# Kernel tuning notes

Measured on AMD Instinct MI355X. Metric: run time of the kernel, lower is better.

## Reference

```python
import jax, jax.numpy as jnp
import numpy as np

C = 256          # channels
NH = 8           # heads
DH = 64          # dim_head
NMEM = 4         # num_mem_kv
HIDDEN = NH * DH # 512
SCALE = DH ** (-0.5)


def _rmsnorm(x, gain):
    # F.normalize(x, dim=1) * gain * sqrt(C)  (scale-only RMS norm over channel dim)
    n = jnp.sqrt(jnp.sum(x * x, axis=1, keepdims=True))
    return x / jnp.maximum(n, 1e-12) * gain * (x.shape[1] ** 0.5)


def setup_inputs() -> dict:
    key = jax.random.key(0)
    ks = jax.random.split(key, 6)
    B, Hh, Ww = 16, 64, 64
    return {
        "x": jax.random.normal(ks[0], (B, C, Hh, Ww), jnp.float32),
        "gain1": jnp.ones((1, C, 1, 1), jnp.float32),
        "w_qkv": jax.random.normal(ks[1], (3 * HIDDEN, C), jnp.float32) * 0.02,
        "mem_kv": jax.random.normal(ks[2], (2, NH, DH, NMEM), jnp.float32),
        "w_out": jax.random.normal(ks[3], (C, HIDDEN), jnp.float32) * 0.02,
        "b_out": jnp.zeros((C,), jnp.float32),
        "gain2": jnp.ones((1, C, 1, 1), jnp.float32),
    }


def reference(x, gain1, w_qkv, mem_kv, w_out, b_out, gain2):
    B, _, Hh, Ww = x.shape
    N = Hh * Ww
    # pre-norm
    xn = _rmsnorm(x, gain1)
    # 1x1 conv QKV projection (no bias) == channel GEMM
    qkv = jnp.einsum('oc,bchw->bohw', w_qkv, xn)          # [B, 3*hidden, H, W]
    qkv = qkv.reshape(B, 3, NH, DH, N)                    # chunk + 'b (h c) x y -> b h c (x y)'
    q, k, v = qkv[:, 0], qkv[:, 1], qkv[:, 2]             # [B, h, d, N]
    # learned global memory kv, broadcast over batch
    mem_k = jnp.broadcast_to(mem_kv[0], (B, NH, DH, NMEM))
    mem_v = jnp.broadcast_to(mem_kv[1], (B, NH, DH, NMEM))
    k = jnp.concatenate([mem_k, k], axis=-1)              # [B, h, d, NMEM+N]
    v = jnp.concatenate([mem_v, v], axis=-1)
    # dual softmax: q over feature dim d, k over token dim n
    q = jax.nn.softmax(q, axis=-2) * SCALE
    k = jax.nn.softmax(k, axis=-1)
    # linear attention: O(N) context
    context = jnp.einsum('bhdn,bhen->bhde', k, v)         # [B, h, d, e]
    out = jnp.einsum('bhde,bhdn->bhen', context, q)       # [B, h, e, N]
    out = out.reshape(B, HIDDEN, Hh, Ww)
    # 1x1 conv out projection (with bias) + post RMSNorm
    out = jnp.einsum('oc,bchw->bohw', w_out, out) + b_out[None, :, None, None]
    return _rmsnorm(out, gain2)
```

## Files before the change

### kernel.cpp

```cpp
#include <hip/hip_runtime.h>

typedef __attribute__((ext_vector_type(8))) short bf16x8;
typedef __attribute__((ext_vector_type(4))) short bf16x4;
typedef __attribute__((ext_vector_type(4))) float f32x4;
typedef unsigned short u16;

constexpr int B_   = 16;
constexpr int C_   = 256;
constexpr int NH   = 8;
constexpr int DH   = 64;
constexpr int NMEM = 4;
constexpr int HID  = 512;
constexpr int QKVC = 1536;
constexpr int N_   = 4096;
constexpr int CTXS = 4224;

__device__ __forceinline__ u16 f2b(float f) {
  union { float f; unsigned u; } v{f};
  unsigned r = v.u + 0x7fff + ((v.u >> 16) & 1);
  return (u16)(r >> 16);
}
__device__ __forceinline__ float b2f(u16 h) {
  union { unsigned u; float f; } v; v.u = ((unsigned)h) << 16; return v.f;
}

__device__ __forceinline__ void gld_lds16(const u16* g, u16* l) {
  __builtin_amdgcn_global_load_lds(
      (const __attribute__((address_space(1))) unsigned*)g,
      (__attribute__((address_space(3))) unsigned*)l, 16, 0, 0);
}

__global__ void k_cvtw(const float* __restrict__ wq, const float* __restrict__ wo,
                       u16* __restrict__ wqb, u16* __restrict__ wob) {
  int i = blockIdx.x * 256 + threadIdx.x;
  for (int idx = i; idx < QKVC * C_; idx += gridDim.x * 256) wqb[idx] = f2b(wq[idx]);
  for (int idx = i; idx < C_ * HID; idx += gridDim.x * 256) wob[idx] = f2b(wo[idx]);
}

__global__ __launch_bounds__(256) void k_rms1(const float* __restrict__ x,
                                              const float* __restrict__ g1,
                                              u16* __restrict__ xbT) {
  int g = blockIdx.y;
  int n = blockIdx.x * 64 + (threadIdx.x & 63);
  int ch = threadIdx.x >> 6;
  __shared__ float ssp[4][64];
  __shared__ float invs[64];
  const float* xp = x + (size_t)g * C_ * N_ + n;
  float ss = 0.f;
  #pragma unroll 16
  for (int c = ch * 64; c < ch * 64 + 64; ++c) {
    float v = xp[(size_t)c * N_];
    ss += v * v;
  }
  ssp[ch][n & 63] = ss;
  __syncthreads();
  if (threadIdx.x < 64) {
    float tot = (ssp[0][threadIdx.x] + ssp[1][threadIdx.x]) +
                (ssp[2][threadIdx.x] + ssp[3][threadIdx.x]);
    invs[threadIdx.x] = 16.0f / fmaxf(sqrtf(tot), 1e-12f);
  }
  __syncthreads();
  float inv = invs[n & 63];
  u16* op = xbT + ((size_t)g * N_ + n) * C_;
  #pragma unroll 2
  for (int c0 = ch * 64; c0 < ch * 64 + 64; c0 += 8) {
    union { bf16x8 v; u16 u[8]; } pk;
    #pragma unroll
    for (int j = 0; j < 8; ++j) pk.u[j] = f2b(xp[(size_t)(c0 + j) * N_] * inv * g1[c0 + j]);
    *(bf16x8*)(op + c0) = pk.v;
  }
}

__global__ __launch_bounds__(256) void k_kvctx(const u16* __restrict__ Wb,
                                               const u16* __restrict__ XT,
                                               float* __restrict__ ctxp) {
  __shared__ __align__(16) u16 smem[16384];
  u16* Ws = smem;
  u16* Xs = smem + 8192;
  u16* Pl = smem;
  u16* Vl = smem + 8192;

  int cpx = gridDim.x >> 3;
  int bid = blockIdx.x;
  int L = (bid & 7) * cpx + (bid >> 3);
  int h = L & 7, nc = (L >> 3) & 7, g = L >> 6;
  int t = threadIdx.x, wave = t >> 6, lane = t & 63;
  int wm = wave >> 1, wn = wave & 1;
  int kg = lane >> 4, lr = lane & 15;

  const u16* WK = Wb + (size_t)(HID + h * DH) * C_;
  const u16* WV = Wb + (size_t)(2 * HID + h * DH) * C_;
  const u16* Xg = XT + ((size_t)g * N_ + nc * 512) * C_;

  int rl8 = lane >> 3;
  int cs8 = (lane & 7) ^ rl8;
  const u16* Wsrc = (wave < 2) ? WK : WV;

  f32x4 acc2[4];
  #pragma unroll
  for (int nf = 0; nf < 4; ++nf) acc2[nf] = (f32x4)0.f;
  float rs[4] = {0.f, 0.f, 0.f, 0.f};

  for (int it = 0; it < 4; ++it) {
    f32x4 acc[4][4];
    #pragma unroll
    for (int i = 0; i < 4; ++i)
      #pragma unroll
      for (int j = 0; j < 4; ++j) acc[i][j] = (f32x4)0.f;

    for (int k0 = 0; k0 < C_; k0 += 64) {
      #pragma unroll
      for (int q = 0; q < 4; ++q) {
        int rb = wave * 32 + q * 8;
        int rw = (rb & 63) + rl8;
        int rx = it * 128 + rb + rl8;
        gld_lds16(Wsrc + (size_t)rw * C_ + k0 + cs8 * 8, Ws + rb * 64);
        gld_lds16(Xg + (size_t)rx * C_ + k0 + cs8 * 8, Xs + rb * 64);
      }
      __syncthreads();
      #pragma unroll
      for (int ks = 0; ks < 2; ++ks) {
        int ch = ks * 4 + kg;
        bf16x8 a[4], bv[4];
        #pragma unroll
        for (int mf = 0; mf < 4; ++mf) {
          int r = wm * 64 + mf * 16 + lr;
          a[mf] = *(const bf16x8*)(Xs + r * 64 + ((ch ^ (r & 7)) * 8));
        }
        #pragma unroll
        for (int nf = 0; nf < 4; ++nf) {
          int r = wn * 64 + nf * 16 + lr;
          bv[nf] = *(const bf16x8*)(Ws + r * 64 + ((ch ^ (r & 7)) * 8));
        }
        #pragma unroll
        for (int mf = 0; mf < 4; ++mf)
          #pragma unroll
          for (int nf = 0; nf < 4; ++nf)
            acc[mf][nf] = __builtin_amdgcn_mfma_f32_16x16x32_bf16(a[mf], bv[nf], acc[mf][nf], 0, 0, 0);
      }
      __syncthreads();
    }

    if (wn == 0) {
      #pragma unroll
      for (int mf = 0; mf < 4; ++mf) {
        int nb = wm * 64 + mf * 16 + kg * 4;
        int cc = nb >> 3, off = nb & 7;
        #pragma unroll
        for (int nf = 0; nf < 4; ++nf) {
          int d = nf * 16 + lr;
          float e0 = __expf(acc[mf][nf][0]);
          float e1 = __expf(acc[mf][nf][1]);
          float e2 = __expf(acc[mf][nf][2]);
          float e3 = __expf(acc[mf][nf][3]);
          rs[nf] += (e0 + e1) + (e2 + e3);
          union { bf16x4 v; u16 u[4]; } pk;
          pk.u[0] = f2b(e0); pk.u[1] = f2b(e1); pk.u[2] = f2b(e2); pk.u[3] = f2b(e3);
          *(bf16x4*)(Pl + d * 128 + ((cc ^ (d & 15)) * 8) + off) = pk.v;
        }
      }
    } else {
      #pragma unroll
      for (int mf = 0; mf < 4; ++mf) {
        int nb = wm * 64 + mf * 16 + kg * 4;
        int cc = nb >> 3, off = nb & 7;
        #pragma unroll
        for (int nf = 0; nf < 4; ++nf) {
          int e = nf * 16 + lr;
          union { bf16x4 v; u16 u[4]; } pk;
          pk.u[0] = f2b(acc[mf][nf][0]); pk.u[1] = f2b(acc[mf][nf][1]);
          pk.u[2] = f2b(acc[mf][nf][2]); pk.u[3] = f2b(acc[mf][nf][3]);
          *(bf16x4*)(Vl + e * 128 + ((cc ^ (e & 15)) * 8) + off) = pk.v;
        }
      }
    }
    __syncthreads();

    #pragma unroll
    for (int k = 0; k < 4; ++k) {
      int c = k * 4 + kg;
      bf16x8 af = *(const bf16x8*)(Pl + (wave * 16 + lr) * 128 + ((c ^ lr) * 8));
      #pragma unroll
      for (int nf = 0; nf < 4; ++nf) {
        bf16x8 bfv = *(const bf16x8*)(Vl + (nf * 16 + lr) * 128 + ((c ^ lr) * 8));
        acc2[nf] = __builtin_amdgcn_mfma_f32_16x16x32_bf16(af, bfv, acc2[nf], 0, 0, 0);
      }
    }
    __syncthreads();
  }

  float* cgp = ctxp + ((size_t)(g * NH + h) * 8 + nc) * CTXS;
  #pragma unroll
  for (int nf = 0; nf < 4; ++nf)
    #pragma unroll
    for (int j = 0; j < 4; ++j) {
      int d = wave * 16 + kg * 4 + j;
      int e = nf * 16 + lr;
      cgp[d * 64 + e] = acc2[nf][j];
    }
  if (wn == 0) {
    #pragma unroll
    for (int nf = 0; nf < 4; ++nf) {
      rs[nf] += __shfl_xor(rs[nf], 16);
      rs[nf] += __shfl_xor(rs[nf], 32);
    }
    if (lane < 16) {
      #pragma unroll
      for (int nf = 0; nf < 4; ++nf)
        cgp[4096 + wm * 64 + nf * 16 + lane] = rs[nf];
    }
  }
}

__global__ __launch_bounds__(256) void k_cwo(const float* __restrict__ ctxp,
                                             const float* __restrict__ memkv,
                                             const u16* __restrict__ Wo,
                                             u16* __restrict__ wo2) {
  int g = blockIdx.y, h = blockIdx.x;
  int t = threadIdx.x, wave = t >> 6, lane = t & 63;
  int kg = lane >> 4, lr = lane & 15;
  int rl8 = lane >> 3, cs8 = (lane & 7) ^ rl8;
  __shared__ float emk[DH * NMEM];
  __shared__ float sd[DH];
  __shared__ __align__(16) u16 Cl[64 * 64];
  __shared__ __align__(16) u16 As2[256 * 64];

  const float* mk = memkv + (size_t)h * DH * NMEM;
  const float* mv = memkv + (size_t)(NH + h) * DH * NMEM;
  const float* cp = ctxp + (size_t)(g * NH + h) * 8 * CTXS;
  emk[t] = __expf(mk[t]);
  __syncthreads();
  if (t < DH) {
    float s = 0.f;
    #pragma unroll
    for (int p = 0; p < 8; ++p)
      s += cp[p * CTXS + 4096 + t] + cp[p * CTXS + 4160 + t];
    #pragma unroll
    for (int j = 0; j < NMEM; ++j) s += emk[t * 4 + j];
    sd[t] = s;
  }
  #pragma unroll
  for (int q = 0; q < 8; ++q) {
    int rb = wave * 64 + q * 8;
    gld_lds16(Wo + (size_t)(rb + rl8) * HID + h * DH + cs8 * 8, As2 + rb * 64);
  }
  __syncthreads();
  #pragma unroll
  for (int i = 0; i < 16; ++i) {
    int idx = t + 256 * i;
    int d = idx >> 6, e = idx & 63;
    float v = 0.f;
    #pragma unroll
    for (int p = 0; p < 8; ++p) v += cp[p * CTXS + idx];
    #pragma unroll
    for (int j = 0; j < NMEM; ++j) v += emk[d * 4 + j] * mv[e * 4 + j];
    Cl[d * 64 + (((e >> 3) ^ (d & 7)) * 8) + (e & 7)] = f2b(v / sd[d]);
  }
  __syncthreads();
  f32x4 acc[4][4];
  #pragma unroll
  for (int i = 0; i < 4; ++i)
    #pragma unroll
    for (int j = 0; j < 4; ++j) acc[i][j] = (f32x4)0.f;
  #pragma unroll
  for (int ks = 0; ks < 2; ++ks) {
    int ch = ks * 4 + kg;
    bf16x8 a[4], b[4];
    #pragma unroll
    for (int mf = 0; mf < 4; ++mf) {
      int r = wave * 64 + mf * 16 + lr;
      a[mf] = *(const bf16x8*)(As2 + r * 64 + ((ch ^ (r & 7)) * 8));
    }
    #pragma unroll
    for (int nf = 0; nf < 4; ++nf) {
      int rd = nf * 16 + lr;
      b[nf] = *(const bf16x8*)(Cl + rd * 64 + ((ch ^ (rd & 7)) * 8));
    }
    #pragma unroll
    for (int mf = 0; mf < 4; ++mf)
      #pragma unroll
      for (int nf = 0; nf < 4; ++nf)
        acc[mf][nf] = __builtin_amdgcn_mfma_f32_16x16x32_bf16(a[mf], b[nf], acc[mf][nf], 0, 0, 0);
  }
  u16* og = wo2 + (size_t)g * 256 * 512;
  #pragma unroll
  for (int mf = 0; mf < 4; ++mf)
    #pragma unroll
    for (int nf = 0; nf < 4; ++nf)
      #pragma unroll
      for (int j = 0; j < 4; ++j) {
        int c = wave * 64 + mf * 16 + kg * 4 + j;
        int dd = nf * 16 + lr;
        og[(size_t)c * 512 + h * DH + dd] = f2b(acc[mf][nf][j]);
      }
}

__global__ __launch_bounds__(512) void k_qout(const u16* __restrict__ Wq,
                                              const u16* __restrict__ XT,
                                              const u16* __restrict__ Wo2,
                                              const float* __restrict__ bias,
                                              const float* __restrict__ g2,
                                              float* __restrict__ out) {
  __shared__ __align__(16) u16 smem[49152];
  u16* R0 = smem;
  u16* R1 = smem + 16384;

  int cpx = gridDim.x >> 3;
  int bid = blockIdx.x;
  int L = (bid & 7) * cpx + (bid >> 3);
  int nc = L & 31, g = L >> 5;
  int t = threadIdx.x, wave = t >> 6, lane = t & 63;
  int kg = lane >> 4, lr = lane & 15;
  int rl4 = lane >> 2, cs4 = (lane & 3) ^ (rl4 & 3);
  int rl8 = lane >> 3, cs8 = (lane & 7) ^ rl8;

  const u16* Xg = XT + ((size_t)g * N_ + nc * 128) * C_;
  const u16* W2g = Wo2 + (size_t)g * 256 * 512;

  {
    int xrow_off = lane >> 5;
    int c32 = lane & 31;
    #pragma unroll
    for (int q = 0; q < 8; ++q) {
      int base = wave * 16 + q * 2;
      int row = base + xrow_off;
      int sw = (c32 & 24) | ((c32 & 7) ^ (row & 7));
      gld_lds16(Xg + (size_t)row * C_ + sw * 8, R1 + base * 256);
    }
  }

  f32x4 acc[4][8];
  #pragma unroll
  for (int i = 0; i < 4; ++i)
    #pragma unroll
    for (int j = 0; j < 8; ++j) acc[i][j] = (f32x4)0.f;

  for (int k0i = 0; k0i < 8; ++k0i) {
    int k0 = k0i * 32;
    #pragma unroll
    for (int q = 0; q < 4; ++q) {
      int rb = ((wave * 4 + q) & 31) * 16;
      gld_lds16(Wq + (size_t)(rb + rl4) * C_ + k0 + cs4 * 8, R0 + rb * 32);
    }
    __syncthreads();
    bf16x8 a[4], bv[8];
    #pragma unroll
    for (int mf = 0; mf < 4; ++mf) {
      int r = wave * 64 + mf * 16 + lr;
      a[mf] = *(const bf16x8*)(R0 + r * 32 + ((kg ^ (r & 3)) * 8));
    }
    #pragma unroll
    for (int nf = 0; nf < 8; ++nf) {
      int bn = nf * 16 + lr;
      int c32 = k0i * 4 + kg;
      int sw = (c32 & 24) | ((c32 & 7) ^ (bn & 7));
      bv[nf] = *(const bf16x8*)(R1 + bn * 256 + sw * 8);
    }
    #pragma unroll
    for (int mf = 0; mf < 4; ++mf)
      #pragma unroll
      for (int nf = 0; nf < 8; ++nf)
        acc[mf][nf] = __builtin_amdgcn_mfma_f32_16x16x32_bf16(a[mf], bv[nf], acc[mf][nf], 0, 0, 0);
    __syncthreads();
  }

  float colsum[8];
  #pragma unroll
  for (int nf = 0; nf < 8; ++nf) {
    float s = 0.f;
    #pragma unroll
    for (int mf = 0; mf < 4; ++mf)
      #pragma unroll
      for (int j = 0; j < 4; ++j) {
        float e = __expf(acc[mf][nf][j]);
        acc[mf][nf][j] = e;
        s += e;
      }
    colsum[nf] = s;
  }
  #pragma unroll
  for (int nf = 0; nf < 8; ++nf) {
    colsum[nf] += __shfl_xor(colsum[nf], 16);
    colsum[nf] += __shfl_xor(colsum[nf], 32);
    colsum[nf] = 0.125f / colsum[nf];
  }
  unsigned pq[4][8][2];
  #pragma unroll
  for (int nf = 0; nf < 8; ++nf) {
    float invs = colsum[nf];
    #pragma unroll
    for (int mf = 0; mf < 4; ++mf)
      #pragma unroll
      for (int jp = 0; jp < 2; ++jp) {
        u16 lo = f2b(acc[mf][nf][jp * 2] * invs);
        u16 hi = f2b(acc[mf][nf][jp * 2 + 1] * invs);
        pq[mf][nf][jp] = (unsigned)lo | ((unsigned)hi << 16);
      }
  }

  f32x4 acc2[2][8];
  #pragma unroll
  for (int i = 0; i < 2; ++i)
    #pragma unroll
    for (int j = 0; j < 8; ++j) acc2[i][j] = (f32x4)0.f;

  #pragma unroll
  for (int half = 0; half < 2; ++half) {
    if ((wave >> 2) == half) {
      #pragma unroll
      for (int nf = 0; nf < 8; ++nf) {
        int n = nf * 16 + lr;
        #pragma unroll
        for (int mf = 0; mf < 4; ++mf)
          #pragma unroll
          for (int jp = 0; jp < 2; ++jp) {
            int oc = (wave & 3) * 64 + mf * 16 + kg * 4 + jp * 2;
            int c8 = oc >> 3;
            int sw = (c8 & 24) | ((c8 & 7) ^ (n & 7));
            *(unsigned*)(R1 + n * 256 + sw * 8 + (oc & 7)) = pq[mf][nf][jp];
          }
      }
    }
    __syncthreads();
    for (int k0l = 0; k0l < 4; ++k0l) {
      int cb = half * 256 + k0l * 64;
      #pragma unroll
      for (int q = 0; q < 4; ++q) {
        int rb = ((wave * 4 + q) & 31) * 8;
        gld_lds16(W2g + (size_t)(rb + rl8) * 512 + cb + cs8 * 8, R0 + rb * 64);
      }
      __syncthreads();
      #pragma unroll
      for (int ks = 0; ks < 2; ++ks) {
        int ch = ks * 4 + kg;
        bf16x8 a2[2], b2[8];
        #pragma unroll
        for (int mf = 0; mf < 2; ++mf) {
          int r = wave * 32 + mf * 16 + lr;
          a2[mf] = *(const bf16x8*)(R0 + r * 64 + ((ch ^ (r & 7)) * 8));
        }
        #pragma unroll
        for (int nf = 0; nf < 8; ++nf) {
          int bn = nf * 16 + lr;
          int c8 = k0l * 8 + ks * 4 + kg;
          int sw = (c8 & 24) | ((c8 & 7) ^ (bn & 7));
          b2[nf] = *(const bf16x8*)(R1 + bn * 256 + sw * 8);
        }
        #pragma unroll
        for (int mf = 0; mf < 2; ++mf)
          #pragma unroll
          for (int nf = 0; nf < 8; ++nf)
            acc2[mf][nf] = __builtin_amdgcn_mfma_f32_16x16x32_bf16(a2[mf], b2[nf], acc2[mf][nf], 0, 0, 0);
      }
      __syncthreads();
    }
  }

  float colsq[8] = {0.f, 0.f, 0.f, 0.f, 0.f, 0.f, 0.f, 0.f};
  #pragma unroll
  for (int mf = 0; mf < 2; ++mf)
    #pragma unroll
    for (int j = 0; j < 4; ++j) {
      int c = wave * 32 + mf * 16 + kg * 4 + j;
      float bs = bias[c];
      #pragma unroll
      for (int nf = 0; nf < 8; ++nf) {
        float v = acc2[mf][nf][j] + bs;
        acc2[mf][nf][j] = v;
        colsq[nf] += v * v;
      }
    }
  #pragma unroll
  for (int nf = 0; nf < 8; ++nf) {
    colsq[nf] += __shfl_xor(colsq[nf], 16);
    colsq[nf] += __shfl_xor(colsq[nf], 32);
  }
  float* part = (float*)R0;
  if (kg == 0) {
    #pragma unroll
    for (int nf = 0; nf < 8; ++nf) part[wave * 128 + nf * 16 + lr] = colsq[nf];
  }
  __syncthreads();
  float* og = out + (size_t)g * C_ * N_ + nc * 128;
  #pragma unroll
  for (int nf = 0; nf < 8; ++nf) {
    int col = nf * 16 + lr;
    float tot = 0.f;
    #pragma unroll
    for (int w = 0; w < 8; ++w) tot += part[w * 128 + col];
    float invn = 16.0f / fmaxf(sqrtf(tot), 1e-12f);
    #pragma unroll
    for (int mf = 0; mf < 2; ++mf)
      #pragma unroll
      for (int j = 0; j < 4; ++j) {
        int c = wave * 32 + mf * 16 + kg * 4 + j;
        og[(size_t)c * N_ + col] = acc2[mf][nf][j] * invn * g2[c];
      }
  }
}

extern "C" void kernel_launch(void* const* d_in, const int* in_sizes, int n_in,
                              void* d_out, int out_size, void* d_ws, size_t ws_size,
                              hipStream_t stream) {
  (void)in_sizes; (void)n_in; (void)out_size;
  const float* x      = (const float*)d_in[0];
  const float* gain1  = (const float*)d_in[1];
  const float* w_qkv  = (const float*)d_in[2];
  const float* mem_kv = (const float*)d_in[3];
  const float* w_out  = (const float*)d_in[4];
  const float* b_out  = (const float*)d_in[5];
  const float* gain2  = (const float*)d_in[6];
  float* out = (float*)d_out;

  char* ws = (char*)d_ws;
  u16* wqkvb = (u16*)ws;
  u16* woutb = (u16*)(ws + 786432);
  size_t shared_b = 1048576;

  const size_t xbT_b  = (size_t)N_ * C_ * 2;
  const size_t ctxp_b = (size_t)NH * 8 * CTXS * 4;
  const size_t wo2_b  = (size_t)256 * 512 * 2;
  const size_t per_b  = xbT_b + ctxp_b + wo2_b;

  int G = 16;
  while (G > 1 && shared_b + (size_t)G * per_b > ws_size) G >>= 1;

  char* base = ws + shared_b;
  u16*   xbT  = (u16*)base;
  float* ctxp = (float*)(base + (size_t)G * xbT_b);
  u16*   wo2  = (u16*)(base + (size_t)G * (xbT_b + ctxp_b));

  k_cvtw<<<256, 256, 0, stream>>>(w_qkv, w_out, wqkvb, woutb);

  for (int b0 = 0; b0 < B_; b0 += G) {
    const float* xc = x + (size_t)b0 * C_ * N_;
    float*       oc = out + (size_t)b0 * C_ * N_;
    k_rms1  <<<dim3(N_ / 64, G),   256, 0, stream>>>(xc, gain1, xbT);
    k_kvctx <<<dim3(64 * G),       256, 0, stream>>>(wqkvb, xbT, ctxp);
    k_cwo   <<<dim3(NH, G),        256, 0, stream>>>(ctxp, mem_kv, woutb, wo2);
    k_qout  <<<dim3(32 * G),       512, 0, stream>>>(wqkvb, xbT, wo2, b_out, gain2, oc);
  }
}
```

Measured before the change: 164.7 us.

## Register-prefetch weight tiles and use lighter barriers in k_qout

Weight tiles for both GEMMs in k_qout are no longer loaded with direct global-to-LDS copies. Each tile is now prefetched into registers one step ahead and written to LDS with swizzled stores, so the global load latency overlaps with the MFMA work of the current step. __syncthreads is replaced by barriers that wait only on LDS counters, and waves_per_eu is pinned to 2. In exchange, register pressure rises from the extra prefetch registers and the loops are fully unrolled.

```diff
diff --git a/kernel.cpp b/kernel.cpp
--- a/kernel.cpp
+++ b/kernel.cpp
@@ -14,6 +14,9 @@
 constexpr int QKVC = 1536;
 constexpr int N_   = 4096;
 constexpr int CTXS = 4224;
+
+#define SBAR() asm volatile("s_waitcnt lgkmcnt(0)\ns_barrier" ::: "memory")
+#define KBAR() asm volatile("s_waitcnt vmcnt(0) lgkmcnt(0)\ns_barrier" ::: "memory")
 
 __device__ __forceinline__ u16 f2b(float f) {
   union { float f; unsigned u; } v{f};
@@ -295,12 +298,13 @@
       }
 }
 
-__global__ __launch_bounds__(512) void k_qout(const u16* __restrict__ Wq,
-                                              const u16* __restrict__ XT,
-                                              const u16* __restrict__ Wo2,
-                                              const float* __restrict__ bias,
-                                              const float* __restrict__ g2,
-                                              float* __restrict__ out) {
+__global__ __launch_bounds__(512) __attribute__((amdgpu_waves_per_eu(2, 2)))
+void k_qout(const u16* __restrict__ Wq,
+            const u16* __restrict__ XT,
+            const u16* __restrict__ Wo2,
+            const float* __restrict__ bias,
+            const float* __restrict__ g2,
+            float* __restrict__ out) {
   __shared__ __align__(16) u16 smem[49152];
   u16* R0 = smem;
   u16* R1 = smem + 16384;
@@ -311,8 +315,9 @@
   int nc = L & 31, g = L >> 5;
   int t = threadIdx.x, wave = t >> 6, lane = t & 63;
   int kg = lane >> 4, lr = lane & 15;
-  int rl4 = lane >> 2, cs4 = (lane & 3) ^ (rl4 & 3);
-  int rl8 = lane >> 3, cs8 = (lane & 7) ^ rl8;
+  int rl4 = lane >> 2;
+  int rl8 = lane >> 3;
+  int ch4 = lane & 3, ch8 = lane & 7;
 
   const u16* Xg = XT + ((size_t)g * N_ + nc * 128) * C_;
   const u16* W2g = Wo2 + (size_t)g * 256 * 512;
@@ -329,20 +334,41 @@
     }
   }
 
+  bf16x8 wreg[4], wo2reg[4];
+  #pragma unroll
+  for (int q = 0; q < 4; ++q) {
+    int r = ((wave * 4 + q) & 31) * 16 + rl4;
+    wreg[q] = *(const bf16x8*)(Wq + (size_t)r * C_ + ch4 * 8);
+  }
+  KBAR();
+
   f32x4 acc[4][8];
   #pragma unroll
   for (int i = 0; i < 4; ++i)
     #pragma unroll
     for (int j = 0; j < 8; ++j) acc[i][j] = (f32x4)0.f;
 
+  #pragma unroll
   for (int k0i = 0; k0i < 8; ++k0i) {
-    int k0 = k0i * 32;
     #pragma unroll
     for (int q = 0; q < 4; ++q) {
-      int rb = ((wave * 4 + q) & 31) * 16;
-      gld_lds16(Wq + (size_t)(rb + rl4) * C_ + k0 + cs4 * 8, R0 + rb * 32);
-    }
-    __syncthreads();
+      int r = ((wave * 4 + q) & 31) * 16 + rl4;
+      *(bf16x8*)(R0 + r * 32 + ((ch4 ^ (r & 3)) * 8)) = wreg[q];
+    }
+    if (k0i < 7) {
+      #pragma unroll
+      for (int q = 0; q < 4; ++q) {
+        int r = ((wave * 4 + q) & 31) * 16 + rl4;
+        wreg[q] = *(const bf16x8*)(Wq + (size_t)r * C_ + (k0i + 1) * 32 + ch4 * 8);
+      }
+    } else {
+      #pragma unroll
+      for (int q = 0; q < 4; ++q) {
+        int r = ((wave * 4 + q) & 31) * 8 + rl8;
+        wo2reg[q] = *(const bf16x8*)(W2g + (size_t)r * 512 + ch8 * 8);
+      }
+    }
+    SBAR();
     bf16x8 a[4], bv[8];
     #pragma unroll
     for (int mf = 0; mf < 4; ++mf) {
@@ -361,7 +387,7 @@
       #pragma unroll
       for (int nf = 0; nf < 8; ++nf)
         acc[mf][nf] = __builtin_amdgcn_mfma_f32_16x16x32_bf16(a[mf], bv[nf], acc[mf][nf], 0, 0, 0);
-    __syncthreads();
+    SBAR();
   }
 
   float colsum[8];
@@ -421,15 +447,23 @@
           }
       }
     }
-    __syncthreads();
+    SBAR();
+    #pragma unroll
     for (int k0l = 0; k0l < 4; ++k0l) {
-      int cb = half * 256 + k0l * 64;
       #pragma unroll
       for (int q = 0; q < 4; ++q) {
-        int rb = ((wave * 4 + q) & 31) * 8;
-        gld_lds16(W2g + (size_t)(rb + rl8) * 512 + cb + cs8 * 8, R0 + rb * 64);
-      }
-      __syncthreads();
+        int r = ((wave * 4 + q) & 31) * 8 + rl8;
+        *(bf16x8*)(R0 + r * 64 + ((ch8 ^ (r & 7)) * 8)) = wo2reg[q];
+      }
+      if (half * 4 + k0l < 7) {
+        int cbn = (half * 4 + k0l + 1) * 64;
+        #pragma unroll
+        for (int q = 0; q < 4; ++q) {
+          int r = ((wave * 4 + q) & 31) * 8 + rl8;
+          wo2reg[q] = *(const bf16x8*)(W2g + (size_t)r * 512 + cbn + ch8 * 8);
+        }
+      }
+      SBAR();
       #pragma unroll
       for (int ks = 0; ks < 2; ++ks) {
         int ch = ks * 4 + kg;
@@ -452,7 +486,7 @@
           for (int nf = 0; nf < 8; ++nf)
             acc2[mf][nf] = __builtin_amdgcn_mfma_f32_16x16x32_bf16(a2[mf], b2[nf], acc2[mf][nf], 0, 0, 0);
       }
-      __syncthreads();
+      SBAR();
     }
   }
 
```

Result: faster. 161.4 us (-2.0%).
